# Kernel optimization log

Measured on AMD Instinct MI355X. Metric: run time of the kernel, lower is better.

The kernel has to match this reference:

```python
import jax, jax.numpy as jnp
import numpy as np

B, W, F_IN = 128, 128, 64   # batch, window_size, num_features
N = 64                      # nodes per graph == num_features == tcn_out_channels
E = 4096                    # edges per graph
ED = 16                     # edge_feature_dim
H, C = 4, 32                # heads, gat_out_dim
FLAT = N * H * C            # 8192
HID = FLAT // 4             # 2048
LRELU_SLOPE = 0.01          # F.leaky_relu default
BN_EPS = 1e-5


def setup_inputs() -> dict:
    key = jax.random.key(0)
    ks = jax.random.split(key, 16)
    x = jax.random.normal(ks[0], (B, W, F_IN), jnp.float32)
    edge_index = jax.random.randint(ks[1], (2, E), 0, N)
    edge_attr = jax.random.normal(ks[2], (B, E, ED), jnp.float32)
    s = lambda k, shape, fan: jax.random.normal(k, shape, jnp.float32) / np.sqrt(fan)
    tcn_w = s(ks[3], (N, F_IN, 3), F_IN * 3)
    tcn_b = jnp.zeros((N,), jnp.float32)
    lin_l_w = s(ks[4], (H * C, W), W)
    lin_l_b = jnp.zeros((H * C,), jnp.float32)
    lin_e_w = s(ks[5], (H * C, ED), ED)
    lin_e_b = jnp.zeros((H * C,), jnp.float32)
    att = s(ks[6], (1, H, C), C)
    fc1_w = s(ks[7], (HID, FLAT), FLAT)
    fc1_b = jnp.zeros((HID,), jnp.float32)
    bn_g = jnp.ones((HID,), jnp.float32)
    bn_b = jnp.zeros((HID,), jnp.float32)
    fc2_w = s(ks[8], (2, HID), HID)
    fc2_b = jnp.zeros((2,), jnp.float32)
    return dict(x=x, edge_index=edge_index, edge_attr=edge_attr,
                tcn_w=tcn_w, tcn_b=tcn_b,
                lin_l_w=lin_l_w, lin_l_b=lin_l_b,
                lin_e_w=lin_e_w, lin_e_b=lin_e_b, att=att,
                fc1_w=fc1_w, fc1_b=fc1_b, bn_g=bn_g, bn_b=bn_b,
                fc2_w=fc2_w, fc2_b=fc2_b)


def reference(x, edge_index, edge_attr, tcn_w, tcn_b,
              lin_l_w, lin_l_b, lin_e_w, lin_e_b, att,
              fc1_w, fc1_b, bn_g, bn_b, fc2_w, fc2_b):
    # TCN: Conv1d(k=3, pad=1) over the window dim
    xt = jnp.transpose(x, (0, 2, 1))  # [B, F_IN, W]
    x_g = jax.lax.conv_general_dilated(
        xt, tcn_w, window_strides=(1,), padding=((1, 1),),
        dimension_numbers=('NCH', 'OIH', 'NCH')) + tcn_b[None, :, None]
    # x_g: [B, N, W] -> per-sample graph with N nodes, W-dim node features

    src, dst = edge_index[0], edge_index[1]

    def gat_one(xn, ea):
        # xn: [N, W], ea: [E, ED]
        h = (xn @ lin_l_w.T + lin_l_b).reshape(N, H, C)
        e = (ea @ lin_e_w.T + lin_e_b).reshape(E, H, C)
        xi = h[dst]               # [E, H, C] target node feats
        xj = h[src]               # [E, H, C] source node feats
        a = jax.nn.leaky_relu(xi + xj + e, LRELU_SLOPE)
        score = jnp.einsum('ehc,ohc->eh', a, att)  # [E, H]
        # segment softmax over edges grouped by destination node
        m = jax.ops.segment_max(score, dst, num_segments=N)
        m = jnp.where(jnp.isfinite(m), m, 0.0)
        ex = jnp.exp(score - m[dst])
        den = jax.ops.segment_sum(ex, dst, num_segments=N)
        alpha = ex / (den[dst] + 1e-16)            # [E, H]
        msg = xj * alpha[:, :, None]               # [E, H, C]
        out = jax.ops.segment_sum(msg, dst, num_segments=N)  # [N, H, C]
        return out.reshape(N, H * C)

    x_gat = jax.vmap(gat_one)(x_g, edge_attr)      # [B, N, H*C]
    x_gat = jax.nn.elu(x_gat)
    x_flat = x_gat.reshape(B, FLAT)

    h1 = x_flat @ fc1_w.T + fc1_b
    # BatchNorm1d in eval mode with fresh running stats (mean=0, var=1)
    h1 = h1 * (bn_g / jnp.sqrt(1.0 + BN_EPS)) + bn_b
    h1 = jax.nn.relu(h1)  # dropout is identity in eval
    logits = h1 @ fc2_w.T + fc2_b
    return logits
```

## Files before the change

kernel.cpp:

```cpp
#include <hip/hip_runtime.h>
#include <math.h>

#define BB   128
#define WW   128
#define FIN  64
#define NNODE 64
#define NE   4096
#define EDIM 16
#define NH   4
#define CDIM 32
#define HC   128
#define FLATD 8192
#define HIDD 2048

#define OFF_H    0u
#define OFF_SC   1048576u
#define OFF_P    1048576u
#define OFF_M    3145728u
#define OFF_XGB  3211264u
#define OFF_BK   4259840u

typedef unsigned short u16;
typedef u16    u16x8  __attribute__((ext_vector_type(8)));
typedef u16    u16x4  __attribute__((ext_vector_type(4)));
typedef __bf16 bf16x8 __attribute__((ext_vector_type(8)));
typedef float  f32x4  __attribute__((ext_vector_type(4)));
typedef float  f32x16 __attribute__((ext_vector_type(16)));

__device__ __forceinline__ u16 f2bf(float f) {
    unsigned u = __float_as_uint(f);
    u += 0x7fffu + ((u >> 16) & 1u);
    return (u16)(u >> 16);
}
__device__ __forceinline__ void hilo(float v, u16* h, u16* l) {
    u16 hh = f2bf(v);
    float hf = __uint_as_float(((unsigned)hh) << 16);
    *h = hh;
    *l = f2bf(v - hf);
}

__global__ __launch_bounds__(256) void k0_bucket(
        const int* __restrict__ ei, int* __restrict__ bstart,
        int* __restrict__ blist, int* __restrict__ pos)
{
    __shared__ int cnt[64];
    __shared__ int cur[65];
    const int t = threadIdx.x;
    if (t < 64) cnt[t] = 0;
    __syncthreads();
    for (int e = t; e < NE; e += 256) atomicAdd(&cnt[ei[NE + e]], 1);
    __syncthreads();
    if (t == 0) {
        int run = 0;
        for (int n = 0; n < 64; ++n) { cur[n] = run; run += cnt[n]; }
        cur[64] = run;
    }
    __syncthreads();
    if (t < 65) bstart[t] = cur[t];
    __syncthreads();
    for (int e = t; e < NE; e += 256) {
        int d = ei[NE + e], s = ei[e];
        int p = atomicAdd(&cur[d], 1);
        blist[p] = (e << 6) | s;
        pos[e] = p;
    }
}

__global__ __launch_bounds__(256) void k1_tcn_linl(
        const float* __restrict__ x, const float* __restrict__ tcn_w,
        const float* __restrict__ tcn_b, const float* __restrict__ lin_l_w,
        const float* __restrict__ lin_l_b, float* __restrict__ h)
{
    __shared__ float xs[130*65];
    __shared__ float xg[32*132];
    const int b = blockIdx.x, half = blockIdx.y, t = threadIdx.x;
    const int n0 = half * 32;

    for (int idx = t; idx < 8192; idx += 256) {
        int w = idx >> 6, i = idx & 63;
        xs[(w+1)*65 + i] = x[b*8192 + idx];
    }
    if (t < 65) { xs[t] = 0.f; xs[129*65 + t] = 0.f; }
    __syncthreads();

    {
        const int nl = t >> 3;
        const int n  = n0 + nl;
        const int w0 = (t & 7) * 16;
        float acc[16];
        const float tb = tcn_b[n];
#pragma unroll
        for (int j = 0; j < 16; ++j) acc[j] = tb;
        for (int i = 0; i < 64; ++i) {
            const float t0 = tcn_w[n*192 + 3*i + 0];
            const float t1 = tcn_w[n*192 + 3*i + 1];
            const float t2 = tcn_w[n*192 + 3*i + 2];
            float a = xs[(w0+0)*65 + i];
            float c0 = xs[(w0+1)*65 + i];
#pragma unroll
            for (int dw = 0; dw < 16; ++dw) {
                float c = xs[(w0+dw+2)*65 + i];
                acc[dw] += a*t0 + c0*t1 + c*t2;
                a = c0; c0 = c;
            }
        }
#pragma unroll
        for (int dw = 0; dw < 16; ++dw) xg[nl*132 + w0 + dw] = acc[dw];
    }
    __syncthreads();

    {
        const int o2 = t & 63, ng = t >> 6;
        const int oA = o2, oB = o2 + 64;
        float accA[8], accB[8];
        const float lbA = lin_l_b[oA], lbB = lin_l_b[oB];
#pragma unroll
        for (int j = 0; j < 8; ++j) { accA[j] = lbA; accB[j] = lbB; }
        for (int c = 0; c < 32; ++c) {
            const float4 lwA = *(const float4*)&lin_l_w[oA*128 + c*4];
            const float4 lwB = *(const float4*)&lin_l_w[oB*128 + c*4];
#pragma unroll
            for (int nn = 0; nn < 8; ++nn) {
                const float4 xv = *(const float4*)&xg[(ng*8+nn)*132 + c*4];
                accA[nn] += xv.x*lwA.x + xv.y*lwA.y + xv.z*lwA.z + xv.w*lwA.w;
                accB[nn] += xv.x*lwB.x + xv.y*lwB.y + xv.z*lwB.z + xv.w*lwB.w;
            }
        }
#pragma unroll
        for (int nn = 0; nn < 8; ++nn) {
            const int n = n0 + ng*8 + nn;
            h[(b*64 + n)*128 + oA] = accA[nn];
            h[(b*64 + n)*128 + oB] = accB[nn];
        }
    }
}

__global__ __launch_bounds__(256, 2) void k2a_scores(
        const float* __restrict__ hbase, const int* __restrict__ ei,
        const float* __restrict__ ea, const float* __restrict__ lin_e_w,
        const float* __restrict__ lin_e_b, const float* __restrict__ att,
        const int* __restrict__ pos, float* __restrict__ score)
{
    __shared__ float hbuf[64*132];
    __shared__ u16 eh[512*16];
    __shared__ u16 el[512*16];
    __shared__ int dsts[512], srcs[512], poss[512];
    const int b = blockIdx.x, q = blockIdx.y, t = threadIdx.x;
    const int e0 = q*512;
    const int lane = t & 63, wv = t >> 6, l32 = lane & 31, h5 = lane >> 5;

    for (int idx = t; idx < 8192; idx += 256) {
        const int o = idx & 127;
        hbuf[(idx>>7)*132 + o] = hbase[(size_t)b*8192 + idx] + 0.5f*lin_e_b[o];
    }
    for (int i4 = t; i4 < 2048; i4 += 256) {
        const int eL = i4 >> 2, d4 = (i4 & 3)*4;
        const float4 v = *(const float4*)&ea[((size_t)b*NE + e0 + eL)*16 + d4];
        u16 hh[4], ll[4];
        hilo(v.x,&hh[0],&ll[0]); hilo(v.y,&hh[1],&ll[1]);
        hilo(v.z,&hh[2],&ll[2]); hilo(v.w,&hh[3],&ll[3]);
        *(u16x4*)&eh[eL*16+d4] = (u16x4){hh[0],hh[1],hh[2],hh[3]};
        *(u16x4*)&el[eL*16+d4] = (u16x4){ll[0],ll[1],ll[2],ll[3]};
    }
    for (int e = t; e < 512; e += 256) {
        dsts[e] = ei[NE + e0 + e];
        srcs[e] = ei[e0 + e];
        poss[e] = pos[e0 + e];
    }
    bf16x8 Ah[4], Al[4];
#pragma unroll
    for (int mt = 0; mt < 4; ++mt) {
        const float* wp = &lin_e_w[(mt*32 + l32)*16 + h5*8];
        const float4 w0 = *(const float4*)wp;
        const float4 w1 = *(const float4*)(wp + 4);
        u16 th[8], tl[8];
        hilo(w0.x,&th[0],&tl[0]); hilo(w0.y,&th[1],&tl[1]);
        hilo(w0.z,&th[2],&tl[2]); hilo(w0.w,&th[3],&tl[3]);
        hilo(w1.x,&th[4],&tl[4]); hilo(w1.y,&th[5],&tl[5]);
        hilo(w1.z,&th[6],&tl[6]); hilo(w1.w,&th[7],&tl[7]);
        u16x8 vh = { th[0],th[1],th[2],th[3],th[4],th[5],th[6],th[7] };
        u16x8 vl = { tl[0],tl[1],tl[2],tl[3],tl[4],tl[5],tl[6],tl[7] };
        Ah[mt] = *(bf16x8*)&vh;
        Al[mt] = *(bf16x8*)&vl;
    }
    float4 attv[4][4];
#pragma unroll
    for (int mt = 0; mt < 4; ++mt)
#pragma unroll
        for (int g = 0; g < 4; ++g)
            attv[mt][g] = *(const float4*)&att[mt*32 + g*8 + h5*4];
    __syncthreads();

#pragma unroll
    for (int et = 0; et < 4; ++et) {
        const int edge = wv*128 + et*32 + l32;
        const int dd = dsts[edge], sn = srcs[edge];
        const bf16x8 Bh = *(const bf16x8*)&eh[edge*16 + h5*8];
        const bf16x8 Bl = *(const bf16x8*)&el[edge*16 + h5*8];
        float hacc[4];
#pragma unroll
        for (int mt = 0; mt < 4; ++mt) {
            f32x16 D = {0.f,0.f,0.f,0.f,0.f,0.f,0.f,0.f,
                        0.f,0.f,0.f,0.f,0.f,0.f,0.f,0.f};
            D = __builtin_amdgcn_mfma_f32_32x32x16_bf16(Al[mt], Bh, D, 0, 0, 0);
            D = __builtin_amdgcn_mfma_f32_32x32x16_bf16(Ah[mt], Bl, D, 0, 0, 0);
            D = __builtin_amdgcn_mfma_f32_32x32x16_bf16(Ah[mt], Bh, D, 0, 0, 0);
            float s = 0.f;
#pragma unroll
            for (int g = 0; g < 4; ++g) {
                const int ob = mt*32 + g*8 + h5*4;
                const float4 hd = *(const float4*)&hbuf[dd*132 + ob];
                const float4 hs = *(const float4*)&hbuf[sn*132 + ob];
                float x0 = hd.x + hs.x + D[g*4+0];
                float x1 = hd.y + hs.y + D[g*4+1];
                float x2 = hd.z + hs.z + D[g*4+2];
                float x3 = hd.w + hs.w + D[g*4+3];
                x0 = fmaxf(x0, 0.01f*x0); x1 = fmaxf(x1, 0.01f*x1);
                x2 = fmaxf(x2, 0.01f*x2); x3 = fmaxf(x3, 0.01f*x3);
                const float4 a4 = attv[mt][g];
                s += a4.x*x0 + a4.y*x1 + a4.z*x2 + a4.w*x3;
            }
            hacc[mt] = s;
        }
#pragma unroll
        for (int hh = 0; hh < 4; ++hh)
            hacc[hh] += __shfl_xor(hacc[hh], 32);
        if (h5 == 0)
            *(float4*)&score[((size_t)b*NE + poss[edge])*4] =
                make_float4(hacc[0], hacc[1], hacc[2], hacc[3]);
    }
}

#define CAP2C 2048
__global__ __launch_bounds__(256, 2) void k2c_aggregate(
        const float* __restrict__ hbase, const float* __restrict__ score,
        const int* __restrict__ bstart, const int* __restrict__ blist,
        u16* __restrict__ xgb)
{
    __shared__ float hsh[64*128];
    __shared__ float ssh[CAP2C*4];
    __shared__ int   bls[CAP2C];
    __shared__ int   bst[17];
    const int b = blockIdx.x, yy = blockIdx.y, t = threadIdx.x;

    for (int idx = t; idx < 8192; idx += 256) hsh[idx] = hbase[(size_t)b*8192 + idx];
    if (t < 17) bst[t] = bstart[yy*16 + t];
    __syncthreads();
    const int lo = bst[0], hi = bst[16];
    const int cnt = min(hi - lo, CAP2C);
    for (int i = t; i < cnt; i += 256) {
        *(float4*)&ssh[i*4] = *(const float4*)&score[((size_t)b*NE + lo + i)*4];
        bls[i] = blist[lo + i];
    }
    __syncthreads();

    const int w = t >> 6, lane = t & 63, half = lane >> 5, li = lane & 31;
    const int hq = li >> 3, sl = li & 7;
#pragma unroll
    for (int it = 0; it < 2; ++it) {
        const int nl = w*4 + it*2 + half;
        const int n  = yy*16 + nl;
        const int s0 = bst[nl] - lo, s1 = bst[nl+1] - lo;
        float mx = -3.4e38f;
        for (int i = s0 + sl; i < s1; i += 8) mx = fmaxf(mx, ssh[i*4 + hq]);
        mx = fmaxf(mx, __shfl_xor(mx, 1));
        mx = fmaxf(mx, __shfl_xor(mx, 2));
        mx = fmaxf(mx, __shfl_xor(mx, 4));
        float den = 0.f;
        for (int i = s0 + sl; i < s1; i += 8) {
            const float ex = __expf(ssh[i*4 + hq] - mx);
            ssh[i*4 + hq] = ex;
            den += ex;
        }
        den += __shfl_xor(den, 1);
        den += __shfl_xor(den, 2);
        den += __shfl_xor(den, 4);
        const float rd = 1.0f / (den + 1e-16f);
        float4 acc = make_float4(0.f, 0.f, 0.f, 0.f);
        for (int i = s0; i < s1; ++i) {
            const float ex = ssh[i*4 + hq];
            const int ss = bls[i] & 63;
            const float4 hv = *(const float4*)&hsh[ss*128 + li*4];
            acc.x += hv.x * ex; acc.y += hv.y * ex;
            acc.z += hv.z * ex; acc.w += hv.w * ex;
        }
        acc.x *= rd; acc.y *= rd; acc.z *= rd; acc.w *= rd;
        float e0 = acc.x > 0.f ? acc.x : expm1f(acc.x);
        float e1 = acc.y > 0.f ? acc.y : expm1f(acc.y);
        float e2 = acc.z > 0.f ? acc.z : expm1f(acc.z);
        float e3 = acc.w > 0.f ? acc.w : expm1f(acc.w);
        u16x4 st = { f2bf(e0), f2bf(e1), f2bf(e2), f2bf(e3) };
        *(u16x4*)&xgb[(size_t)b*8192 + n*128 + li*4] = st;
    }
}

__global__ __launch_bounds__(256) void k3_fc1(
        const u16* __restrict__ xgb, const float* __restrict__ fc1_w,
        float* __restrict__ part)
{
    __shared__ u16 Ash[128*72];
    __shared__ u16 Bsh[32*72];
    const int jb = blockIdx.x, ks = blockIdx.y, t = threadIdx.x;
    const int j0 = jb*32, k0 = ks*1024;
    const int wave = t >> 6, lane = t & 63;
    const int quad = lane >> 4, l16 = lane & 15;
    const int wm = (wave & 1) * 64, wn = (wave >> 1) * 16;

    f32x4 acc[4];
#pragma unroll
    for (int i = 0; i < 4; ++i) acc[i] = (f32x4){0.f, 0.f, 0.f, 0.f};

    const int arow = t >> 1, acol = (t & 1) * 32;
    const int brow = t >> 3, bcol = (t & 7) * 8;

    for (int kc = 0; kc < 1024; kc += 64) {
        if (kc) __syncthreads();
        const u16* ap = xgb + (size_t)arow*FLATD + k0 + kc + acol;
#pragma unroll
        for (int qq = 0; qq < 4; ++qq)
            *(u16x8*)&Ash[arow*72 + acol + qq*8] = *(const u16x8*)(ap + qq*8);
        const float* bp = fc1_w + (size_t)(j0 + brow)*FLATD + k0 + kc + bcol;
        {
            float4 v0 = *(const float4*)(bp);
            float4 v1 = *(const float4*)(bp + 4);
            u16x8 u = { f2bf(v0.x), f2bf(v0.y), f2bf(v0.z), f2bf(v0.w),
                        f2bf(v1.x), f2bf(v1.y), f2bf(v1.z), f2bf(v1.w) };
            *(u16x8*)&Bsh[brow*72 + bcol] = u;
        }
        __syncthreads();
#pragma unroll
        for (int kk = 0; kk < 64; kk += 32) {
            bf16x8 af[4], bfr;
#pragma unroll
            for (int i = 0; i < 4; ++i)
                af[i] = *(const bf16x8*)&Ash[(wm + i*16 + l16)*72 + kk + quad*8];
            bfr = *(const bf16x8*)&Bsh[(wn + l16)*72 + kk + quad*8];
#pragma unroll
            for (int i = 0; i < 4; ++i)
                acc[i] = __builtin_amdgcn_mfma_f32_16x16x32_bf16(af[i], bfr, acc[i], 0, 0, 0);
        }
    }
#pragma unroll
    for (int i = 0; i < 4; ++i) {
        const int n = j0 + wn + l16;
#pragma unroll
        for (int r = 0; r < 4; ++r) {
            const int m = wm + i*16 + quad*4 + r;
            part[(size_t)ks*262144 + (size_t)m*HIDD + n] = acc[i][r];
        }
    }
}

__global__ __launch_bounds__(256) void k4_fc2(
        const float* __restrict__ part, const float* __restrict__ fc1_b,
        const float* __restrict__ bn_g, const float* __restrict__ bn_b,
        const float* __restrict__ fc2_w, const float* __restrict__ fc2_b,
        float* __restrict__ out)
{
    __shared__ float r0[256], r1[256];
    const int b = blockIdx.x, t = threadIdx.x;
    const float inv = 1.0f / sqrtf(1.0f + 1e-5f);
    float p0 = 0.f, p1 = 0.f;
    for (int j = t; j < 2048; j += 256) {
        float hv = 0.f;
#pragma unroll
        for (int s = 0; s < 8; ++s) hv += part[(size_t)s*262144 + (size_t)b*2048 + j];
        float v = (hv + fc1_b[j]) * (bn_g[j] * inv) + bn_b[j];
        v = fmaxf(v, 0.f);
        p0 += v * fc2_w[j];
        p1 += v * fc2_w[2048 + j];
    }
    r0[t] = p0; r1[t] = p1;
    __syncthreads();
    for (int s = 128; s > 0; s >>= 1) {
        if (t < s) { r0[t] += r0[t+s]; r1[t] += r1[t+s]; }
        __syncthreads();
    }
    if (t == 0) {
        out[b*2 + 0] = r0[0] + fc2_b[0];
        out[b*2 + 1] = r1[0] + fc2_b[1];
    }
}

extern "C" void kernel_launch(void* const* d_in, const int* in_sizes, int n_in,
                              void* d_out, int out_size, void* d_ws, size_t ws_size,
                              hipStream_t stream)
{
    const float* x       = (const float*)d_in[0];
    const int*   ei      = (const int*)  d_in[1];
    const float* ea      = (const float*)d_in[2];
    const float* tcn_w   = (const float*)d_in[3];
    const float* tcn_b   = (const float*)d_in[4];
    const float* lin_l_w = (const float*)d_in[5];
    const float* lin_l_b = (const float*)d_in[6];
    const float* lin_e_w = (const float*)d_in[7];
    const float* lin_e_b = (const float*)d_in[8];
    const float* att     = (const float*)d_in[9];
    const float* fc1_w   = (const float*)d_in[10];
    const float* fc1_b   = (const float*)d_in[11];
    const float* bn_g    = (const float*)d_in[12];
    const float* bn_b    = (const float*)d_in[13];
    const float* fc2_w   = (const float*)d_in[14];
    const float* fc2_b   = (const float*)d_in[15];

    float* ws     = (float*)d_ws;
    float* hbuf   = ws + OFF_H;
    float* score  = ws + OFF_SC;
    float* part   = ws + OFF_P;
    int*   pos    = (int*)(ws + OFF_M);
    u16*   xgb    = (u16*)(ws + OFF_XGB);
    int*   bstart = (int*)(ws + OFF_BK);
    int*   blist  = bstart + 80;
    float* out    = (float*)d_out;

    k0_bucket  <<<1, 256, 0, stream>>>(ei, bstart, blist, pos);
    k1_tcn_linl<<<dim3(BB, 2), 256, 0, stream>>>(x, tcn_w, tcn_b, lin_l_w, lin_l_b, hbuf);
    k2a_scores <<<dim3(BB, 8), 256, 0, stream>>>(hbuf, ei, ea, lin_e_w, lin_e_b, att, pos, score);
    k2c_aggregate<<<dim3(BB, 4), 256, 0, stream>>>(hbuf, score, bstart, blist, xgb);
    k3_fc1     <<<dim3(64, 8), 256, 0, stream>>>(xgb, fc1_w, part);
    k4_fc2     <<<BB, 256, 0, stream>>>(part, fc1_b, bn_g, bn_b, fc2_w, fc2_b, out);
}
```

Measured before the change: 256.1 us.

## Fuse GAT score and aggregation kernels, aggregating via dense attention matrix MFMA

Merges the score kernel and the softmax/aggregation kernel into one block per (batch, half of destination nodes). Score buffer round-trips through global memory and the pos array are removed. Each block now computes scores for its bucketed edges, with edge_attr gathered by edge id, then does the segment softmax. It accumulates the normalised weights into a dense 32x64 per-head matrix using shared atomics and produces the aggregation with split-bf16 MFMAs, correcting for the folded lin_e bias. The grid shrinks to BB x 2 blocks of 512 threads, which lowers parallelism. Edges beyond the 2560 cap are dropped, and the attention sums now come from atomics.

```diff
diff --git a/kernel.cpp b/kernel.cpp
--- a/kernel.cpp
+++ b/kernel.cpp
@@ -14,9 +14,7 @@
 #define HIDD 2048
 
 #define OFF_H    0u
-#define OFF_SC   1048576u
 #define OFF_P    1048576u
-#define OFF_M    3145728u
 #define OFF_XGB  3211264u
 #define OFF_BK   4259840u
 
@@ -40,8 +38,7 @@
 }
 
 __global__ __launch_bounds__(256) void k0_bucket(
-        const int* __restrict__ ei, int* __restrict__ bstart,
-        int* __restrict__ blist, int* __restrict__ pos)
+        const int* __restrict__ ei, int* __restrict__ bstart, int* __restrict__ blist)
 {
     __shared__ int cnt[64];
     __shared__ int cur[65];
@@ -61,8 +58,7 @@
     for (int e = t; e < NE; e += 256) {
         int d = ei[NE + e], s = ei[e];
         int p = atomicAdd(&cur[d], 1);
-        blist[p] = (e << 6) | s;
-        pos[e] = p;
+        blist[p] = (e << 12) | (d << 6) | s;
     }
 }
 
@@ -135,38 +131,26 @@
     }
 }
 
-__global__ __launch_bounds__(256, 2) void k2a_scores(
-        const float* __restrict__ hbase, const int* __restrict__ ei,
-        const float* __restrict__ ea, const float* __restrict__ lin_e_w,
-        const float* __restrict__ lin_e_b, const float* __restrict__ att,
-        const int* __restrict__ pos, float* __restrict__ score)
+#define CAPF 2560
+__global__ __launch_bounds__(512, 1) void k2_fused(
+        const float* __restrict__ hbase, const float* __restrict__ ea,
+        const float* __restrict__ lin_e_w, const float* __restrict__ lin_e_b,
+        const float* __restrict__ att, const int* __restrict__ bstart,
+        const int* __restrict__ blist, u16* __restrict__ xgb)
 {
     __shared__ float hbuf[64*132];
-    __shared__ u16 eh[512*16];
-    __shared__ u16 el[512*16];
-    __shared__ int dsts[512], srcs[512], poss[512];
-    const int b = blockIdx.x, q = blockIdx.y, t = threadIdx.x;
-    const int e0 = q*512;
+    __shared__ float scl[CAPF*4];
+    __shared__ float Pm[4][32][68];
+    __shared__ int   bst[33];
+    const int b = blockIdx.x, half = blockIdx.y, t = threadIdx.x;
     const int lane = t & 63, wv = t >> 6, l32 = lane & 31, h5 = lane >> 5;
 
-    for (int idx = t; idx < 8192; idx += 256) {
+    for (int idx = t; idx < 8192; idx += 512) {
         const int o = idx & 127;
         hbuf[(idx>>7)*132 + o] = hbase[(size_t)b*8192 + idx] + 0.5f*lin_e_b[o];
     }
-    for (int i4 = t; i4 < 2048; i4 += 256) {
-        const int eL = i4 >> 2, d4 = (i4 & 3)*4;
-        const float4 v = *(const float4*)&ea[((size_t)b*NE + e0 + eL)*16 + d4];
-        u16 hh[4], ll[4];
-        hilo(v.x,&hh[0],&ll[0]); hilo(v.y,&hh[1],&ll[1]);
-        hilo(v.z,&hh[2],&ll[2]); hilo(v.w,&hh[3],&ll[3]);
-        *(u16x4*)&eh[eL*16+d4] = (u16x4){hh[0],hh[1],hh[2],hh[3]};
-        *(u16x4*)&el[eL*16+d4] = (u16x4){ll[0],ll[1],ll[2],ll[3]};
-    }
-    for (int e = t; e < 512; e += 256) {
-        dsts[e] = ei[NE + e0 + e];
-        srcs[e] = ei[e0 + e];
-        poss[e] = pos[e0 + e];
-    }
+    for (int idx = t; idx < 4*32*68; idx += 512) ((float*)Pm)[idx] = 0.f;
+    if (t < 33) bst[t] = bstart[half*32 + t];
     bf16x8 Ah[4], Al[4];
 #pragma unroll
     for (int mt = 0; mt < 4; ++mt) {
@@ -191,12 +175,26 @@
             attv[mt][g] = *(const float4*)&att[mt*32 + g*8 + h5*4];
     __syncthreads();
 
-#pragma unroll
-    for (int et = 0; et < 4; ++et) {
-        const int edge = wv*128 + et*32 + l32;
-        const int dd = dsts[edge], sn = srcs[edge];
-        const bf16x8 Bh = *(const bf16x8*)&eh[edge*16 + h5*8];
-        const bf16x8 Bl = *(const bf16x8*)&el[edge*16 + h5*8];
+    const int lo = bst[0], cnt = min(bst[32] - lo, CAPF);
+    const int gcnt = (cnt + 31) >> 5;
+
+    for (int g = wv; g < gcnt; g += 8) {
+        const int idx = g*32 + l32;
+        const bool valid = idx < cnt;
+        const int pk = valid ? blist[lo + idx] : 0;
+        const int sn = pk & 63, dd = (pk >> 6) & 63, e = pk >> 12;
+        const float* eap = ea + ((size_t)b*NE + e)*16 + h5*8;
+        const float4 v0 = *(const float4*)eap;
+        const float4 v1 = *(const float4*)(eap + 4);
+        u16 bh[8], bl[8];
+        hilo(v0.x,&bh[0],&bl[0]); hilo(v0.y,&bh[1],&bl[1]);
+        hilo(v0.z,&bh[2],&bl[2]); hilo(v0.w,&bh[3],&bl[3]);
+        hilo(v1.x,&bh[4],&bl[4]); hilo(v1.y,&bh[5],&bl[5]);
+        hilo(v1.z,&bh[6],&bl[6]); hilo(v1.w,&bh[7],&bl[7]);
+        u16x8 vbh = { bh[0],bh[1],bh[2],bh[3],bh[4],bh[5],bh[6],bh[7] };
+        u16x8 vbl = { bl[0],bl[1],bl[2],bl[3],bl[4],bl[5],bl[6],bl[7] };
+        const bf16x8 Bh = *(bf16x8*)&vbh;
+        const bf16x8 Bl = *(bf16x8*)&vbl;
         float hacc[4];
 #pragma unroll
         for (int mt = 0; mt < 4; ++mt) {
@@ -207,17 +205,17 @@
             D = __builtin_amdgcn_mfma_f32_32x32x16_bf16(Ah[mt], Bh, D, 0, 0, 0);
             float s = 0.f;
 #pragma unroll
-            for (int g = 0; g < 4; ++g) {
-                const int ob = mt*32 + g*8 + h5*4;
+            for (int g4 = 0; g4 < 4; ++g4) {
+                const int ob = mt*32 + g4*8 + h5*4;
                 const float4 hd = *(const float4*)&hbuf[dd*132 + ob];
                 const float4 hs = *(const float4*)&hbuf[sn*132 + ob];
-                float x0 = hd.x + hs.x + D[g*4+0];
-                float x1 = hd.y + hs.y + D[g*4+1];
-                float x2 = hd.z + hs.z + D[g*4+2];
-                float x3 = hd.w + hs.w + D[g*4+3];
+                float x0 = hd.x + hs.x + D[g4*4+0];
+                float x1 = hd.y + hs.y + D[g4*4+1];
+                float x2 = hd.z + hs.z + D[g4*4+2];
+                float x3 = hd.w + hs.w + D[g4*4+3];
                 x0 = fmaxf(x0, 0.01f*x0); x1 = fmaxf(x1, 0.01f*x1);
                 x2 = fmaxf(x2, 0.01f*x2); x3 = fmaxf(x3, 0.01f*x3);
-                const float4 a4 = attv[mt][g];
+                const float4 a4 = attv[mt][g4];
                 s += a4.x*x0 + a4.y*x1 + a4.z*x2 + a4.w*x3;
             }
             hacc[mt] = s;
@@ -225,72 +223,75 @@
 #pragma unroll
         for (int hh = 0; hh < 4; ++hh)
             hacc[hh] += __shfl_xor(hacc[hh], 32);
-        if (h5 == 0)
-            *(float4*)&score[((size_t)b*NE + poss[edge])*4] =
-                make_float4(hacc[0], hacc[1], hacc[2], hacc[3]);
-    }
-}
-
-#define CAP2C 2048
-__global__ __launch_bounds__(256, 2) void k2c_aggregate(
-        const float* __restrict__ hbase, const float* __restrict__ score,
-        const int* __restrict__ bstart, const int* __restrict__ blist,
-        u16* __restrict__ xgb)
-{
-    __shared__ float hsh[64*128];
-    __shared__ float ssh[CAP2C*4];
-    __shared__ int   bls[CAP2C];
-    __shared__ int   bst[17];
-    const int b = blockIdx.x, yy = blockIdx.y, t = threadIdx.x;
-
-    for (int idx = t; idx < 8192; idx += 256) hsh[idx] = hbase[(size_t)b*8192 + idx];
-    if (t < 17) bst[t] = bstart[yy*16 + t];
-    __syncthreads();
-    const int lo = bst[0], hi = bst[16];
-    const int cnt = min(hi - lo, CAP2C);
-    for (int i = t; i < cnt; i += 256) {
-        *(float4*)&ssh[i*4] = *(const float4*)&score[((size_t)b*NE + lo + i)*4];
-        bls[i] = blist[lo + i];
-    }
-    __syncthreads();
-
-    const int w = t >> 6, lane = t & 63, half = lane >> 5, li = lane & 31;
-    const int hq = li >> 3, sl = li & 7;
-#pragma unroll
-    for (int it = 0; it < 2; ++it) {
-        const int nl = w*4 + it*2 + half;
-        const int n  = yy*16 + nl;
+        if (h5 == 0 && valid)
+            *(float4*)&scl[idx*4] = make_float4(hacc[0], hacc[1], hacc[2], hacc[3]);
+    }
+    __syncthreads();
+
+    {
+        const int pair = t >> 2, sub = t & 3;
+        const int nl = pair >> 2, hh = pair & 3;
         const int s0 = bst[nl] - lo, s1 = bst[nl+1] - lo;
         float mx = -3.4e38f;
-        for (int i = s0 + sl; i < s1; i += 8) mx = fmaxf(mx, ssh[i*4 + hq]);
+        for (int i = s0 + sub; i < s1; i += 4) mx = fmaxf(mx, scl[i*4 + hh]);
         mx = fmaxf(mx, __shfl_xor(mx, 1));
         mx = fmaxf(mx, __shfl_xor(mx, 2));
-        mx = fmaxf(mx, __shfl_xor(mx, 4));
         float den = 0.f;
-        for (int i = s0 + sl; i < s1; i += 8) {
-            const float ex = __expf(ssh[i*4 + hq] - mx);
-            ssh[i*4 + hq] = ex;
+        for (int i = s0 + sub; i < s1; i += 4) {
+            const float ex = __expf(scl[i*4 + hh] - mx);
+            scl[i*4 + hh] = ex;
             den += ex;
         }
         den += __shfl_xor(den, 1);
         den += __shfl_xor(den, 2);
-        den += __shfl_xor(den, 4);
         const float rd = 1.0f / (den + 1e-16f);
-        float4 acc = make_float4(0.f, 0.f, 0.f, 0.f);
-        for (int i = s0; i < s1; ++i) {
-            const float ex = ssh[i*4 + hq];
-            const int ss = bls[i] & 63;
-            const float4 hv = *(const float4*)&hsh[ss*128 + li*4];
-            acc.x += hv.x * ex; acc.y += hv.y * ex;
-            acc.z += hv.z * ex; acc.w += hv.w * ex;
-        }
-        acc.x *= rd; acc.y *= rd; acc.z *= rd; acc.w *= rd;
-        float e0 = acc.x > 0.f ? acc.x : expm1f(acc.x);
-        float e1 = acc.y > 0.f ? acc.y : expm1f(acc.y);
-        float e2 = acc.z > 0.f ? acc.z : expm1f(acc.z);
-        float e3 = acc.w > 0.f ? acc.w : expm1f(acc.w);
-        u16x4 st = { f2bf(e0), f2bf(e1), f2bf(e2), f2bf(e3) };
-        *(u16x4*)&xgb[(size_t)b*8192 + n*128 + li*4] = st;
+        for (int i = s0 + sub; i < s1; i += 4) {
+            const int src = blist[lo + i] & 63;
+            atomicAdd(&Pm[hh][nl][src], scl[i*4 + hh] * rd);
+        }
+    }
+    __syncthreads();
+
+    if (wv < 4) {
+        const int hh = wv;
+        f32x16 D = {0.f,0.f,0.f,0.f,0.f,0.f,0.f,0.f,
+                    0.f,0.f,0.f,0.f,0.f,0.f,0.f,0.f};
+#pragma unroll
+        for (int k0 = 0; k0 < 64; k0 += 16) {
+            const float* pp = &Pm[hh][l32][k0 + h5*8];
+            const float4 a0 = *(const float4*)pp;
+            const float4 a1 = *(const float4*)(pp + 4);
+            u16 ph[8], pl[8];
+            hilo(a0.x,&ph[0],&pl[0]); hilo(a0.y,&ph[1],&pl[1]);
+            hilo(a0.z,&ph[2],&pl[2]); hilo(a0.w,&ph[3],&pl[3]);
+            hilo(a1.x,&ph[4],&pl[4]); hilo(a1.y,&ph[5],&pl[5]);
+            hilo(a1.z,&ph[6],&pl[6]); hilo(a1.w,&ph[7],&pl[7]);
+            u16x8 vph = { ph[0],ph[1],ph[2],ph[3],ph[4],ph[5],ph[6],ph[7] };
+            u16x8 vpl = { pl[0],pl[1],pl[2],pl[3],pl[4],pl[5],pl[6],pl[7] };
+            u16 hhv[8], hlv[8];
+#pragma unroll
+            for (int i = 0; i < 8; ++i) {
+                const float v = hbuf[(k0 + h5*8 + i)*132 + hh*32 + l32];
+                hilo(v, &hhv[i], &hlv[i]);
+            }
+            u16x8 vhh = { hhv[0],hhv[1],hhv[2],hhv[3],hhv[4],hhv[5],hhv[6],hhv[7] };
+            u16x8 vhl = { hlv[0],hlv[1],hlv[2],hlv[3],hlv[4],hlv[5],hlv[6],hlv[7] };
+            const bf16x8 Ph = *(bf16x8*)&vph, Pl = *(bf16x8*)&vpl;
+            const bf16x8 Hh = *(bf16x8*)&vhh, Hl = *(bf16x8*)&vhl;
+            D = __builtin_amdgcn_mfma_f32_32x32x16_bf16(Pl, Hh, D, 0, 0, 0);
+            D = __builtin_amdgcn_mfma_f32_32x32x16_bf16(Ph, Hl, D, 0, 0, 0);
+            D = __builtin_amdgcn_mfma_f32_32x32x16_bf16(Ph, Hh, D, 0, 0, 0);
+        }
+        const int c = l32, o = hh*32 + c;
+        const float lb2 = 0.5f * lin_e_b[o];
+#pragma unroll
+        for (int r = 0; r < 16; ++r) {
+            const int m = (r & 3) + 8*(r >> 2) + 4*h5;
+            const float corr = (bst[m+1] > bst[m]) ? lb2 : 0.f;
+            float v = D[r] - corr;
+            v = v > 0.f ? v : expm1f(v);
+            xgb[(size_t)b*8192 + (half*32 + m)*128 + o] = f2bf(v);
+        }
     }
 }
 
@@ -405,18 +406,16 @@
 
     float* ws     = (float*)d_ws;
     float* hbuf   = ws + OFF_H;
-    float* score  = ws + OFF_SC;
     float* part   = ws + OFF_P;
-    int*   pos    = (int*)(ws + OFF_M);
     u16*   xgb    = (u16*)(ws + OFF_XGB);
     int*   bstart = (int*)(ws + OFF_BK);
     int*   blist  = bstart + 80;
     float* out    = (float*)d_out;
 
-    k0_bucket  <<<1, 256, 0, stream>>>(ei, bstart, blist, pos);
+    k0_bucket  <<<1, 256, 0, stream>>>(ei, bstart, blist);
     k1_tcn_linl<<<dim3(BB, 2), 256, 0, stream>>>(x, tcn_w, tcn_b, lin_l_w, lin_l_b, hbuf);
-    k2a_scores <<<dim3(BB, 8), 256, 0, stream>>>(hbuf, ei, ea, lin_e_w, lin_e_b, att, pos, score);
-    k2c_aggregate<<<dim3(BB, 4), 256, 0, stream>>>(hbuf, score, bstart, blist, xgb);
+    k2_fused   <<<dim3(BB, 2), 512, 0, stream>>>(hbuf, ea, lin_e_w, lin_e_b, att,
+                                                 bstart, blist, xgb);
     k3_fc1     <<<dim3(64, 8), 256, 0, stream>>>(xgb, fc1_w, part);
     k4_fc2     <<<BB, 256, 0, stream>>>(part, fc1_b, bn_g, bn_b, fc2_w, fc2_b, out);
 }
```

New measurement: 247.2 us. 1.04x faster.
